# Performance work log

Hardware: AMD Instinct MI355X
Metric: run time of the kernel (lower is better)

## Reference

```python
import jax, jax.numpy as jnp
import numpy as np

B, H, S, D = 2, 12, 1024, 128
KQ, KK = 6, 11  # per-head conv kernel over (query, key) score plane


def setup_inputs() -> dict:
    key = jax.random.key(0)
    kq, kk, kv, kw = jax.random.split(key, 4)
    Q = jax.random.normal(kq, (B, H, S, D), dtype=jnp.float32)
    K = jax.random.normal(kk, (B, H, S, D), dtype=jnp.float32)
    V = jax.random.normal(kv, (B, H, S, D), dtype=jnp.float32)
    W = jax.random.normal(kw, (H, KQ, KK), dtype=jnp.float32) * 0.1
    return {"Q": Q, "K": K, "V": V, "W": W}


def reference(Q, K, V, W):
    # causal=True, softmax_scale = 1/sqrt(head_dim)  (module defaults)
    b, h, s, d = Q.shape
    _, kq, kk = W.shape
    pad_q = kq - 1            # causal padding along the query axis
    pad_k = (kk - 1) // 2     # 'same' padding along the key axis
    scale = 1.0 / np.sqrt(d).astype(np.float32)

    # Raw QK^T scores: [b, h, s_q, s_k]
    scores = jnp.einsum('bhqd,bhkd->bhqk', Q, K)

    # Causal: zero out future keys before the conv so the kernel cannot mix
    # in future information (matches the `causal` flag passed into the
    # fused qk_conv kernel; out-of-range tiles load as 0 in the Triton code).
    tril = jnp.tril(jnp.ones((s, s), dtype=bool))
    scores = jnp.where(tril[None, None], scores, 0.0)

    # Per-head 2D conv over the (q, k) plane: grouped conv with H groups,
    # kernel W[h] applied to head h's score map. Cross-correlation (PyTorch
    # conv semantics == lax.conv_general_dilated without kernel flip).
    conv = jax.lax.conv_general_dilated(
        scores,                      # [b, h, s, s] as NCHW
        W[:, None, :, :],            # [h, 1, kq, kk] as OIHW, groups=h
        window_strides=(1, 1),
        padding=((pad_q, 0), (pad_k, pad_k)),
        feature_group_count=h,
        dimension_numbers=('NCHW', 'OIHW', 'NCHW'),
    )

    # Scale, re-apply causal mask with the kernel's -1e6 fill, softmax, @V.
    logits = conv * scale + jnp.where(tril[None, None], 0.0, -1000000.0)
    P = jax.nn.softmax(logits, axis=-1)
    O = jnp.einsum('bhqk,bhkd->bhqd', P, V)
    return O
```

## Files before the change

### kernel.cpp

```cpp
#include <hip/hip_runtime.h>
#include <hip/hip_bf16.h>
#include <math.h>

#define B_ 2
#define H_ 12
#define S_ 1024
#define D_ 128
#define TQ 32
#define TK 32
#define NW 4
#define SCALE 0.08838834764831843f

#define QPAD 16
#define QROWS (S_ + QPAD)
#define KPAD 16
#define KROWS (KPAD + S_ + 16)

typedef __attribute__((ext_vector_type(8))) short short8;
typedef __attribute__((ext_vector_type(4))) float floatx4;

__device__ __forceinline__ float b2f(short s) {
    unsigned int x = ((unsigned int)(unsigned short)s) << 16;
    return __builtin_bit_cast(float, x);
}
__device__ __forceinline__ unsigned short f2b(float f) {
    return __builtin_bit_cast(unsigned short, __float2bfloat16(f));
}

__global__ __launch_bounds__(256) void cvt_pad_kernel(
    const float* __restrict__ src, unsigned short* __restrict__ dst,
    int rows_total)
{
    int idx = blockIdx.x * 256 + threadIdx.x;
    size_t e0 = (size_t)idx * 4;
    int bh = (int)(e0 / ((size_t)rows_total * D_));
    int rem = (int)(e0 - (size_t)bh * rows_total * D_);
    int r = rem / D_;
    int d = rem - r * D_;
    int sr = r - 16;
    float4 v = make_float4(0.f, 0.f, 0.f, 0.f);
    if (sr >= 0 && sr < S_)
        v = *(const float4*)(src + ((size_t)bh * S_ + sr) * D_ + d);
    ushort4 o;
    o.x = f2b(v.x); o.y = f2b(v.y); o.z = f2b(v.z); o.w = f2b(v.w);
    *(ushort4*)(dst + ((size_t)bh * rows_total + r) * D_ + d) = o;
}

__global__ __launch_bounds__(256) void vt_kernel(
    const float* __restrict__ V, unsigned short* __restrict__ Vt)
{
    __shared__ float ls[32][33];
    int b = blockIdx.x;
    int dt = b & 3; int kt = (b >> 2) & 31; int bh = b >> 7;
    int t = threadIdx.x;
    int lk = t >> 3, ld = (t & 7) * 4;
    float4 v = *(const float4*)(V + ((size_t)bh * S_ + kt * 32 + lk) * D_ + dt * 32 + ld);
    ls[lk][ld + 0] = v.x; ls[lk][ld + 1] = v.y; ls[lk][ld + 2] = v.z; ls[lk][ld + 3] = v.w;
    __syncthreads();
    int lk2 = t >> 3, lc = (t & 7) * 4;
    ushort4 o;
    o.x = f2b(ls[lc + 0][lk2]); o.y = f2b(ls[lc + 1][lk2]);
    o.z = f2b(ls[lc + 2][lk2]); o.w = f2b(ls[lc + 3][lk2]);
    *(ushort4*)(Vt + ((size_t)bh * D_ + dt * 32 + lk2) * S_ + kt * 32 + lc) = o;
}

__global__ __launch_bounds__(256, 2) void conv_attn_mfma(
    const unsigned short* __restrict__ Qp,
    const unsigned short* __restrict__ Kp,
    const unsigned short* __restrict__ Vt,
    const float* __restrict__ W,
    float* __restrict__ O)
{
    __shared__ __align__(16) union {
        unsigned short sc[NW][48][72];
        float oacc[32][132];
    } u;
    __shared__ float m_all[NW][32], l_all[NW][32], ms_s[32], inv_s[32];

    const int tid = threadIdx.x;
    const int wv = tid >> 6;
    const int ln = tid & 63;
    const int l15 = ln & 15;
    const int qd = ln >> 4;

    const int bid = blockIdx.x;
    const int bh = bid % (B_ * H_);
    const int qt = (S_ / TQ - 1) - bid / (B_ * H_);
    const int h = bh % H_;
    const int q0 = qt * TQ;

    const unsigned short* Qb = Qp + (size_t)bh * QROWS * D_;
    const unsigned short* Kb = Kp + (size_t)bh * KROWS * D_;
    const unsigned short* Vb = Vt + (size_t)bh * D_ * S_;
    const float* Wh = W + h * 66;

    short8 qf[3][4];
    #pragma unroll
    for (int mt = 0; mt < 3; ++mt) {
        const unsigned short* row = Qb + (size_t)(q0 + mt * 16 + l15) * D_;
        #pragma unroll
        for (int kc = 0; kc < 4; ++kc)
            qf[mt][kc] = *(const short8*)(row + kc * 32 + qd * 8);
    }

    floatx4 acc[2][8];
    #pragma unroll
    for (int mt = 0; mt < 2; ++mt)
        #pragma unroll
        for (int nt = 0; nt < 8; ++nt)
            acc[mt][nt] = (floatx4){0.f, 0.f, 0.f, 0.f};
    float m_run[2] = {-INFINITY, -INFINITY};
    float l_run[2] = {0.f, 0.f};

    const int nkt = qt + 1;
    for (int kt = wv; kt < nkt; kt += NW) {
        const int k0 = kt * TK;

        short8 vf[8];
        #pragma unroll
        for (int nt = 0; nt < 8; ++nt)
            vf[nt] = *(const short8*)(Vb + (size_t)(nt * 16 + l15) * S_ + k0 + qd * 8);

        #pragma unroll
        for (int nt = 0; nt < 3; ++nt) {
            const unsigned short* krow = Kb + (size_t)(k0 + 8 + nt * 16 + l15) * D_;
            short8 kf[4];
            #pragma unroll
            for (int kc = 0; kc < 4; ++kc)
                kf[kc] = *(const short8*)(krow + kc * 32 + qd * 8);
            #pragma unroll
            for (int mt = 0; mt < 3; ++mt) {
                floatx4 s = {0.f, 0.f, 0.f, 0.f};
                #pragma unroll
                for (int kc = 0; kc < 4; ++kc)
                    s = __builtin_amdgcn_mfma_f32_16x16x32_bf16(qf[mt][kc], kf[kc], s, 0, 0, 0);
                const int qrow = q0 - 16 + mt * 16 + qd * 4;
                const int kcol = k0 - 8 + nt * 16 + l15;
                #pragma unroll
                for (int reg = 0; reg < 4; ++reg) {
                    float v = (kcol <= qrow + reg) ? s[reg] : 0.f;
                    u.sc[wv][mt * 16 + qd * 4 + reg][nt * 16 + l15] = f2b(v);
                }
            }
        }

        float pl[2][8];
        #pragma unroll
        for (int mt2 = 0; mt2 < 2; ++mt2)
            #pragma unroll
            for (int jj = 0; jj < 8; ++jj) pl[mt2][jj] = 0.f;
        #pragma unroll
        for (int i = 0; i < 6; ++i) {
            const unsigned short* r0 = &u.sc[wv][l15 + 11 + i][qd * 8];
            const unsigned short* r1 = &u.sc[wv][l15 + 27 + i][qd * 8];
            short8 h0 = *(const short8*)(r0);
            short8 h1 = *(const short8*)(r0 + 8);
            short8 h2 = *(const short8*)(r0 + 16);
            short8 g0 = *(const short8*)(r1);
            short8 g1 = *(const short8*)(r1 + 8);
            short8 g2 = *(const short8*)(r1 + 16);
            float x0[24], x1[24];
            #pragma unroll
            for (int m = 0; m < 8; ++m) {
                x0[m] = b2f(h0[m]); x0[8 + m] = b2f(h1[m]); x0[16 + m] = b2f(h2[m]);
                x1[m] = b2f(g0[m]); x1[8 + m] = b2f(g1[m]); x1[16 + m] = b2f(g2[m]);
            }
            #pragma unroll
            for (int j = 0; j < 11; ++j) {
                const float w = Wh[i * 11 + j];
                #pragma unroll
                for (int jj = 0; jj < 8; ++jj) {
                    pl[0][jj] += w * x0[3 + j + jj];
                    pl[1][jj] += w * x1[3 + j + jj];
                }
            }
        }

        float al[2];
        short8 pfrag[2];
        #pragma unroll
        for (int mt2 = 0; mt2 < 2; ++mt2) {
            const int qrow = q0 + l15 + 16 * mt2;
            float lg[8];
            float mx = -1e30f;
            #pragma unroll
            for (int jj = 0; jj < 8; ++jj) {
                const int kcol = k0 + qd * 8 + jj;
                lg[jj] = (kcol <= qrow) ? pl[mt2][jj] * SCALE : -1e30f;
                mx = fmaxf(mx, lg[jj]);
            }
            mx = fmaxf(mx, __shfl_xor(mx, 16));
            mx = fmaxf(mx, __shfl_xor(mx, 32));
            const float nm = fmaxf(m_run[mt2], mx);
            al[mt2] = __expf(m_run[mt2] - nm);
            float sum = 0.f;
            short8 pb;
            #pragma unroll
            for (int jj = 0; jj < 8; ++jj) {
                float p = __expf(lg[jj] - nm);
                sum += p;
                pb[jj] = (short)f2b(p);
            }
            sum += __shfl_xor(sum, 16);
            sum += __shfl_xor(sum, 32);
            l_run[mt2] = l_run[mt2] * al[mt2] + sum;
            m_run[mt2] = nm;
            pfrag[mt2] = pb;
        }

        #pragma unroll
        for (int mt = 0; mt < 2; ++mt) {
            #pragma unroll
            for (int reg = 0; reg < 4; ++reg) {
                const float af = __shfl(al[mt], qd * 4 + reg, 64);
                #pragma unroll
                for (int nt = 0; nt < 8; ++nt)
                    acc[mt][nt][reg] *= af;
            }
        }

        #pragma unroll
        for (int nt = 0; nt < 8; ++nt)
            #pragma unroll
            for (int mt = 0; mt < 2; ++mt)
                acc[mt][nt] = __builtin_amdgcn_mfma_f32_16x16x32_bf16(pfrag[mt], vf[nt], acc[mt][nt], 0, 0, 0);
    }

    if (qd == 0) {
        m_all[wv][l15] = m_run[0]; m_all[wv][l15 + 16] = m_run[1];
        l_all[wv][l15] = l_run[0]; l_all[wv][l15 + 16] = l_run[1];
    }
    __syncthreads();
    if (tid < 32) {
        float ms = -INFINITY;
        #pragma unroll
        for (int w = 0; w < NW; ++w) ms = fmaxf(ms, m_all[w][tid]);
        float ls = 0.f;
        #pragma unroll
        for (int w = 0; w < NW; ++w) ls += __expf(m_all[w][tid] - ms) * l_all[w][tid];
        ms_s[tid] = ms;
        inv_s[tid] = 1.f / ls;
    }
    __syncthreads();
    for (int w = 0; w < NW; ++w) {
        if (wv == w) {
            #pragma unroll
            for (int mt = 0; mt < 2; ++mt) {
                #pragma unroll
                for (int reg = 0; reg < 4; ++reg) {
                    const int row = mt * 16 + qd * 4 + reg;
                    const float f = __expf(m_all[wv][row] - ms_s[row]);
                    #pragma unroll
                    for (int nt = 0; nt < 8; ++nt) {
                        const float val = acc[mt][nt][reg] * f;
                        if (w == 0) u.oacc[row][nt * 16 + l15] = val;
                        else        u.oacc[row][nt * 16 + l15] += val;
                    }
                }
            }
        }
        __syncthreads();
    }

    {
        const int r = tid >> 3;
        const int c0 = (tid & 7) * 16;
        const float inv = inv_s[r];
        float* orow = O + ((size_t)bh * S_ + q0 + r) * D_ + c0;
        #pragma unroll
        for (int g = 0; g < 4; ++g) {
            float4 o;
            o.x = u.oacc[r][c0 + g * 4 + 0] * inv;
            o.y = u.oacc[r][c0 + g * 4 + 1] * inv;
            o.z = u.oacc[r][c0 + g * 4 + 2] * inv;
            o.w = u.oacc[r][c0 + g * 4 + 3] * inv;
            *(float4*)(orow + g * 4) = o;
        }
    }
}

extern "C" void kernel_launch(void* const* d_in, const int* in_sizes, int n_in,
                              void* d_out, int out_size, void* d_ws, size_t ws_size,
                              hipStream_t stream) {
    const float* Q = (const float*)d_in[0];
    const float* K = (const float*)d_in[1];
    const float* V = (const float*)d_in[2];
    const float* W = (const float*)d_in[3];
    float* O = (float*)d_out;

    unsigned short* Qp = (unsigned short*)d_ws;
    unsigned short* Kp = (unsigned short*)((char*)d_ws + 6389760);
    unsigned short* Vt = (unsigned short*)((char*)d_ws + 12877824);

    cvt_pad_kernel<<<dim3((B_ * H_ * QROWS * D_) / 1024), dim3(256), 0, stream>>>(Q, Qp, QROWS);
    cvt_pad_kernel<<<dim3((B_ * H_ * KROWS * D_) / 1024), dim3(256), 0, stream>>>(K, Kp, KROWS);
    vt_kernel<<<dim3(B_ * H_ * (S_ / 32) * (D_ / 32)), dim3(256), 0, stream>>>(V, Vt);

    conv_attn_mfma<<<dim3(B_ * H_ * (S_ / TQ)), dim3(256), 0, stream>>>(Qp, Kp, Vt, W, O);
}
```

Before: 200.7 us.

## Fold per-head conv weights into K, turning conv-attention into a wide matmul

The kernel now absorbs the (q,k) conv into a precomputed 6x-wide key tensor: each key row is convolved with the head's weights along the key axis for each query offset, so the score becomes one MFMA GEMM over a 768-wide contraction with shifted Q rows. Because zeroing the future entries before the conv does not factor out this way, a small correction band (diagonal offsets 0..10) is precomputed from fp32 Q·K dot products and subtracted on the near-diagonal tiles. This removes the per-tile LDS score staging and the scalar conv FMAs. In exchange it adds a large prep pass that writes a 6x-expanded K and more global traffic in the main loop. The three prep kernels are merged into one launch, and block-to-tile mapping and V layout are permuted.

```diff
diff --git a/kernel.cpp b/kernel.cpp
--- a/kernel.cpp
+++ b/kernel.cpp
@@ -6,6 +6,7 @@
 #define H_ 12
 #define S_ 1024
 #define D_ 128
+#define BH_ (B_ * H_)
 #define TQ 32
 #define TK 32
 #define NW 4
@@ -13,68 +14,127 @@
 
 #define QPAD 16
 #define QROWS (S_ + QPAD)
-#define KPAD 16
-#define KROWS (KPAD + S_ + 16)
+#define KHD 768
+
+#define NB_KH   18432
+#define NB_QP   3120
+#define NB_VT   3072
+#define NB_CORR 384
+#define NB_PREP (NB_KH + NB_QP + NB_VT + NB_CORR)
 
 typedef __attribute__((ext_vector_type(8))) short short8;
 typedef __attribute__((ext_vector_type(4))) float floatx4;
 
-__device__ __forceinline__ float b2f(short s) {
-    unsigned int x = ((unsigned int)(unsigned short)s) << 16;
-    return __builtin_bit_cast(float, x);
-}
 __device__ __forceinline__ unsigned short f2b(float f) {
     return __builtin_bit_cast(unsigned short, __float2bfloat16(f));
 }
 
-__global__ __launch_bounds__(256) void cvt_pad_kernel(
-    const float* __restrict__ src, unsigned short* __restrict__ dst,
-    int rows_total)
+__global__ __launch_bounds__(256) void prep_kernel(
+    const float* __restrict__ Q, const float* __restrict__ K,
+    const float* __restrict__ V, const float* __restrict__ W,
+    unsigned short* __restrict__ Qp, unsigned short* __restrict__ Kh,
+    unsigned short* __restrict__ Vp, float* __restrict__ Corr)
 {
-    int idx = blockIdx.x * 256 + threadIdx.x;
-    size_t e0 = (size_t)idx * 4;
-    int bh = (int)(e0 / ((size_t)rows_total * D_));
-    int rem = (int)(e0 - (size_t)bh * rows_total * D_);
-    int r = rem / D_;
-    int d = rem - r * D_;
-    int sr = r - 16;
-    float4 v = make_float4(0.f, 0.f, 0.f, 0.f);
-    if (sr >= 0 && sr < S_)
-        v = *(const float4*)(src + ((size_t)bh * S_ + sr) * D_ + d);
-    ushort4 o;
-    o.x = f2b(v.x); o.y = f2b(v.y); o.z = f2b(v.z); o.w = f2b(v.w);
-    *(ushort4*)(dst + ((size_t)bh * rows_total + r) * D_ + d) = o;
-}
-
-__global__ __launch_bounds__(256) void vt_kernel(
-    const float* __restrict__ V, unsigned short* __restrict__ Vt)
-{
-    __shared__ float ls[32][33];
-    int b = blockIdx.x;
-    int dt = b & 3; int kt = (b >> 2) & 31; int bh = b >> 7;
-    int t = threadIdx.x;
-    int lk = t >> 3, ld = (t & 7) * 4;
-    float4 v = *(const float4*)(V + ((size_t)bh * S_ + kt * 32 + lk) * D_ + dt * 32 + ld);
-    ls[lk][ld + 0] = v.x; ls[lk][ld + 1] = v.y; ls[lk][ld + 2] = v.z; ls[lk][ld + 3] = v.w;
-    __syncthreads();
-    int lk2 = t >> 3, lc = (t & 7) * 4;
-    ushort4 o;
-    o.x = f2b(ls[lc + 0][lk2]); o.y = f2b(ls[lc + 1][lk2]);
-    o.z = f2b(ls[lc + 2][lk2]); o.w = f2b(ls[lc + 3][lk2]);
-    *(ushort4*)(Vt + ((size_t)bh * D_ + dt * 32 + lk2) * S_ + kt * 32 + lc) = o;
+    __shared__ union {
+        float vt_ls[32][33];
+        float band[69][16];
+    } sm;
+    const int blk = blockIdx.x;
+    const int tid = threadIdx.x;
+
+    if (blk < NB_KH) {
+        const int idx = blk * 256 + tid;
+        const int d4 = idx & 31;
+        const int t2 = idx >> 5;
+        const int i  = t2 % 6;
+        const int t3 = t2 / 6;
+        const int k  = t3 & (S_ - 1);
+        const int bh = t3 >> 10;
+        const int h  = bh % H_;
+        const float* Kb = K + (size_t)bh * S_ * D_ + d4 * 4;
+        const float* wrow = W + h * 66 + i * 11;
+        float ax = 0.f, ay = 0.f, az = 0.f, aw = 0.f;
+        #pragma unroll
+        for (int j = 0; j < 11; ++j) {
+            const int kr = k + j - 5;
+            if (kr >= 0 && kr < S_) {
+                const float w = wrow[j] * SCALE;
+                const float4 kv = *(const float4*)(Kb + (size_t)kr * D_);
+                ax += w * kv.x; ay += w * kv.y; az += w * kv.z; aw += w * kv.w;
+            }
+        }
+        ushort4 o; o.x = f2b(ax); o.y = f2b(ay); o.z = f2b(az); o.w = f2b(aw);
+        *(ushort4*)(Kh + (((size_t)bh * S_ + k) * 6 + i) * D_ + d4 * 4) = o;
+    } else if (blk < NB_KH + NB_QP) {
+        const int idx = (blk - NB_KH) * 256 + tid;
+        const size_t e0 = (size_t)idx * 4;
+        const int bh = (int)(e0 / ((size_t)QROWS * D_));
+        const int rem = (int)(e0 - (size_t)bh * QROWS * D_);
+        const int r = rem / D_;
+        const int d = rem - r * D_;
+        const int sr = r - QPAD;
+        float4 v = make_float4(0.f, 0.f, 0.f, 0.f);
+        if (sr >= 0 && sr < S_)
+            v = *(const float4*)(Q + ((size_t)bh * S_ + sr) * D_ + d);
+        ushort4 o; o.x = f2b(v.x); o.y = f2b(v.y); o.z = f2b(v.z); o.w = f2b(v.w);
+        *(ushort4*)(Qp + ((size_t)bh * QROWS + r) * D_ + d) = o;
+    } else if (blk < NB_KH + NB_QP + NB_VT) {
+        const int b2 = blk - (NB_KH + NB_QP);
+        const int dt = b2 & 3, ktl = (b2 >> 2) & 31, bh = b2 >> 7;
+        const int lk = tid >> 3, ld = (tid & 7) * 4;
+        const float4 v4 = *(const float4*)(V + ((size_t)bh * S_ + ktl * 32 + lk) * D_ + dt * 32 + ld);
+        sm.vt_ls[lk][ld + 0] = v4.x; sm.vt_ls[lk][ld + 1] = v4.y;
+        sm.vt_ls[lk][ld + 2] = v4.z; sm.vt_ls[lk][ld + 3] = v4.w;
+        __syncthreads();
+        const int lk2 = tid >> 3, lc = (tid & 7) * 4;
+        const int pb = ((lc >> 3) << 2) | (((lc >> 2) & 1) << 4);
+        ushort4 o;
+        o.x = f2b(sm.vt_ls[pb + 0][lk2]); o.y = f2b(sm.vt_ls[pb + 1][lk2]);
+        o.z = f2b(sm.vt_ls[pb + 2][lk2]); o.w = f2b(sm.vt_ls[pb + 3][lk2]);
+        *(ushort4*)(Vp + ((size_t)bh * D_ + dt * 32 + lk2) * S_ + ktl * 32 + lc) = o;
+    } else {
+        const int cb = blk - (NB_KH + NB_QP + NB_VT);
+        const int bh = cb >> 4, q0c = (cb & 15) * 64;
+        const int h = bh % H_;
+        for (int s = tid; s < 69 * 16; s += 256) {
+            const int r = s >> 4, dsl = s & 15;
+            float v = 0.f;
+            if (dsl < 10) {
+                const int qp = q0c - 5 + r, delta = dsl + 1;
+                if (qp >= 0 && qp + delta < S_) {
+                    const float4* qr = (const float4*)(Q + ((size_t)bh * S_ + qp) * D_);
+                    const float4* kr = (const float4*)(K + ((size_t)bh * S_ + qp + delta) * D_);
+                    #pragma unroll 8
+                    for (int c = 0; c < 32; ++c) {
+                        const float4 a = qr[c], b = kr[c];
+                        v += a.x * b.x + a.y * b.y + a.z * b.z + a.w * b.w;
+                    }
+                }
+            }
+            sm.band[r][dsl] = v;
+        }
+        __syncthreads();
+        for (int e = tid; e < 64 * 16; e += 256) {
+            const int ql = e >> 4, d = e & 15;
+            float v = 0.f;
+            if (d <= 10) {
+                for (int i2 = 0; i2 < 6; ++i2)
+                    for (int j = i2 + d + 1; j < 11; ++j)
+                        v += W[h * 66 + i2 * 11 + j] * SCALE * sm.band[ql + i2][j - i2 - d - 1];
+            }
+            Corr[((size_t)bh << 14) + ((size_t)(q0c + ql) << 4) + d] = v;
+        }
+    }
 }
 
 __global__ __launch_bounds__(256, 2) void conv_attn_mfma(
     const unsigned short* __restrict__ Qp,
-    const unsigned short* __restrict__ Kp,
-    const unsigned short* __restrict__ Vt,
-    const float* __restrict__ W,
+    const unsigned short* __restrict__ Kh,
+    const unsigned short* __restrict__ Vp,
+    const float* __restrict__ Corr,
     float* __restrict__ O)
 {
-    __shared__ __align__(16) union {
-        unsigned short sc[NW][48][72];
-        float oacc[32][132];
-    } u;
+    __shared__ __align__(16) float oacc[32][132];
     __shared__ float m_all[NW][32], l_all[NW][32], ms_s[32], inv_s[32];
 
     const int tid = threadIdx.x;
@@ -84,146 +144,111 @@
     const int qd = ln >> 4;
 
     const int bid = blockIdx.x;
-    const int bh = bid % (B_ * H_);
-    const int qt = (S_ / TQ - 1) - bid / (B_ * H_);
-    const int h = bh % H_;
-    const int q0 = qt * TQ;
-
-    const unsigned short* Qb = Qp + (size_t)bh * QROWS * D_;
-    const unsigned short* Kb = Kp + (size_t)bh * KROWS * D_;
-    const unsigned short* Vb = Vt + (size_t)bh * D_ * S_;
-    const float* Wh = W + h * 66;
-
-    short8 qf[3][4];
-    #pragma unroll
-    for (int mt = 0; mt < 3; ++mt) {
-        const unsigned short* row = Qb + (size_t)(q0 + mt * 16 + l15) * D_;
-        #pragma unroll
-        for (int kc = 0; kc < 4; ++kc)
-            qf[mt][kc] = *(const short8*)(row + kc * 32 + qd * 8);
-    }
+    const int wg  = (bid & 7) * 96 + (bid >> 3);
+    const int bh  = wg >> 5;
+    const int qt  = (S_ / TQ - 1) - (wg & 31);
+    const int q0  = qt * TQ;
+
+    const unsigned short* Qb0 = Qp + ((size_t)bh * QROWS + q0 + 11 + l15) * D_ + qd * 8;
+    const unsigned short* Qb1 = Qb0 + 16 * D_;
+    const unsigned short* Khb = Kh + (size_t)bh * S_ * KHD;
+    const unsigned short* Vb  = Vp + ((size_t)bh * D_ + l15) * S_ + qd * 8;
+    const float* Cb = Corr + ((size_t)bh << 14);
 
     floatx4 acc[2][8];
     #pragma unroll
     for (int mt = 0; mt < 2; ++mt)
         #pragma unroll
-        for (int nt = 0; nt < 8; ++nt)
-            acc[mt][nt] = (floatx4){0.f, 0.f, 0.f, 0.f};
+        for (int nd = 0; nd < 8; ++nd)
+            acc[mt][nd] = (floatx4){0.f, 0.f, 0.f, 0.f};
     float m_run[2] = {-INFINITY, -INFINITY};
     float l_run[2] = {0.f, 0.f};
 
-    const int nkt = qt + 1;
-    for (int kt = wv; kt < nkt; kt += NW) {
+    for (int kt = wv; kt <= qt; kt += NW) {
         const int k0 = kt * TK;
+        const unsigned short* A0 = Khb + (size_t)(k0 + l15) * KHD + qd * 8;
+        const unsigned short* A1 = A0 + 16 * KHD;
 
         short8 vf[8];
         #pragma unroll
-        for (int nt = 0; nt < 8; ++nt)
-            vf[nt] = *(const short8*)(Vb + (size_t)(nt * 16 + l15) * S_ + k0 + qd * 8);
-
-        #pragma unroll
-        for (int nt = 0; nt < 3; ++nt) {
-            const unsigned short* krow = Kb + (size_t)(k0 + 8 + nt * 16 + l15) * D_;
-            short8 kf[4];
-            #pragma unroll
-            for (int kc = 0; kc < 4; ++kc)
-                kf[kc] = *(const short8*)(krow + kc * 32 + qd * 8);
-            #pragma unroll
-            for (int mt = 0; mt < 3; ++mt) {
-                floatx4 s = {0.f, 0.f, 0.f, 0.f};
-                #pragma unroll
-                for (int kc = 0; kc < 4; ++kc)
-                    s = __builtin_amdgcn_mfma_f32_16x16x32_bf16(qf[mt][kc], kf[kc], s, 0, 0, 0);
-                const int qrow = q0 - 16 + mt * 16 + qd * 4;
-                const int kcol = k0 - 8 + nt * 16 + l15;
-                #pragma unroll
-                for (int reg = 0; reg < 4; ++reg) {
-                    float v = (kcol <= qrow + reg) ? s[reg] : 0.f;
-                    u.sc[wv][mt * 16 + qd * 4 + reg][nt * 16 + l15] = f2b(v);
-                }
-            }
-        }
-
-        float pl[2][8];
-        #pragma unroll
-        for (int mt2 = 0; mt2 < 2; ++mt2)
-            #pragma unroll
-            for (int jj = 0; jj < 8; ++jj) pl[mt2][jj] = 0.f;
-        #pragma unroll
-        for (int i = 0; i < 6; ++i) {
-            const unsigned short* r0 = &u.sc[wv][l15 + 11 + i][qd * 8];
-            const unsigned short* r1 = &u.sc[wv][l15 + 27 + i][qd * 8];
-            short8 h0 = *(const short8*)(r0);
-            short8 h1 = *(const short8*)(r0 + 8);
-            short8 h2 = *(const short8*)(r0 + 16);
-            short8 g0 = *(const short8*)(r1);
-            short8 g1 = *(const short8*)(r1 + 8);
-            short8 g2 = *(const short8*)(r1 + 16);
-            float x0[24], x1[24];
-            #pragma unroll
-            for (int m = 0; m < 8; ++m) {
-                x0[m] = b2f(h0[m]); x0[8 + m] = b2f(h1[m]); x0[16 + m] = b2f(h2[m]);
-                x1[m] = b2f(g0[m]); x1[8 + m] = b2f(g1[m]); x1[16 + m] = b2f(g2[m]);
-            }
-            #pragma unroll
-            for (int j = 0; j < 11; ++j) {
-                const float w = Wh[i * 11 + j];
-                #pragma unroll
-                for (int jj = 0; jj < 8; ++jj) {
-                    pl[0][jj] += w * x0[3 + j + jj];
-                    pl[1][jj] += w * x1[3 + j + jj];
-                }
-            }
-        }
-
+        for (int nd = 0; nd < 8; ++nd)
+            vf[nd] = *(const short8*)(Vb + (size_t)nd * 16 * S_ + k0);
+
+        floatx4 sc_[2][2];
+        #pragma unroll
+        for (int nt = 0; nt < 2; ++nt)
+            #pragma unroll
+            for (int mt = 0; mt < 2; ++mt)
+                sc_[nt][mt] = (floatx4){0.f, 0.f, 0.f, 0.f};
+
+        #pragma unroll
+        for (int c = 0; c < 24; ++c) {
+            const short8 a0 = *(const short8*)(A0 + c * 32);
+            const short8 a1 = *(const short8*)(A1 + c * 32);
+            const short8 b0 = *(const short8*)(Qb0 + (c >> 2) * D_ + (c & 3) * 32);
+            const short8 b1 = *(const short8*)(Qb1 + (c >> 2) * D_ + (c & 3) * 32);
+            sc_[0][0] = __builtin_amdgcn_mfma_f32_16x16x32_bf16(a0, b0, sc_[0][0], 0, 0, 0);
+            sc_[0][1] = __builtin_amdgcn_mfma_f32_16x16x32_bf16(a0, b1, sc_[0][1], 0, 0, 0);
+            sc_[1][0] = __builtin_amdgcn_mfma_f32_16x16x32_bf16(a1, b0, sc_[1][0], 0, 0, 0);
+            sc_[1][1] = __builtin_amdgcn_mfma_f32_16x16x32_bf16(a1, b1, sc_[1][1], 0, 0, 0);
+        }
+
+        const bool need_corr = (kt >= qt - 1);
         float al[2];
         short8 pfrag[2];
         #pragma unroll
-        for (int mt2 = 0; mt2 < 2; ++mt2) {
-            const int qrow = q0 + l15 + 16 * mt2;
+        for (int mt = 0; mt < 2; ++mt) {
+            const int qrow = q0 + mt * 16 + l15;
             float lg[8];
             float mx = -1e30f;
             #pragma unroll
-            for (int jj = 0; jj < 8; ++jj) {
-                const int kcol = k0 + qd * 8 + jj;
-                lg[jj] = (kcol <= qrow) ? pl[mt2][jj] * SCALE : -1e30f;
-                mx = fmaxf(mx, lg[jj]);
-            }
+            for (int nt = 0; nt < 2; ++nt)
+                #pragma unroll
+                for (int rg = 0; rg < 4; ++rg) {
+                    const int kcol = k0 + nt * 16 + qd * 4 + rg;
+                    float v = sc_[nt][mt][rg];
+                    if (need_corr) {
+                        const int dd = qrow - kcol;
+                        if (dd >= 0 && dd <= 10) v -= Cb[(qrow << 4) + dd];
+                    }
+                    const int jj = nt * 4 + rg;
+                    lg[jj] = (kcol <= qrow) ? v : -1e30f;
+                    mx = fmaxf(mx, lg[jj]);
+                }
             mx = fmaxf(mx, __shfl_xor(mx, 16));
             mx = fmaxf(mx, __shfl_xor(mx, 32));
-            const float nm = fmaxf(m_run[mt2], mx);
-            al[mt2] = __expf(m_run[mt2] - nm);
+            const float nm = fmaxf(m_run[mt], mx);
+            al[mt] = __expf(m_run[mt] - nm);
             float sum = 0.f;
-            short8 pb;
+            short8 pbv;
             #pragma unroll
             for (int jj = 0; jj < 8; ++jj) {
-                float p = __expf(lg[jj] - nm);
+                const float p = __expf(lg[jj] - nm);
                 sum += p;
-                pb[jj] = (short)f2b(p);
+                pbv[jj] = (short)f2b(p);
             }
             sum += __shfl_xor(sum, 16);
             sum += __shfl_xor(sum, 32);
-            l_run[mt2] = l_run[mt2] * al[mt2] + sum;
-            m_run[mt2] = nm;
-            pfrag[mt2] = pb;
-        }
-
-        #pragma unroll
-        for (int mt = 0; mt < 2; ++mt) {
-            #pragma unroll
-            for (int reg = 0; reg < 4; ++reg) {
-                const float af = __shfl(al[mt], qd * 4 + reg, 64);
+            l_run[mt] = l_run[mt] * al[mt] + sum;
+            m_run[mt] = nm;
+            pfrag[mt] = pbv;
+        }
+
+        #pragma unroll
+        for (int mt = 0; mt < 2; ++mt)
+            #pragma unroll
+            for (int rg = 0; rg < 4; ++rg) {
+                const float af = __shfl(al[mt], qd * 4 + rg, 64);
                 #pragma unroll
-                for (int nt = 0; nt < 8; ++nt)
-                    acc[mt][nt][reg] *= af;
-            }
-        }
-
-        #pragma unroll
-        for (int nt = 0; nt < 8; ++nt)
+                for (int nd = 0; nd < 8; ++nd)
+                    acc[mt][nd][rg] *= af;
+            }
+
+        #pragma unroll
+        for (int nd = 0; nd < 8; ++nd)
             #pragma unroll
             for (int mt = 0; mt < 2; ++mt)
-                acc[mt][nt] = __builtin_amdgcn_mfma_f32_16x16x32_bf16(pfrag[mt], vf[nt], acc[mt][nt], 0, 0, 0);
+                acc[mt][nd] = __builtin_amdgcn_mfma_f32_16x16x32_bf16(pfrag[mt], vf[nd], acc[mt][nd], 0, 0, 0);
     }
 
     if (qd == 0) {
@@ -247,14 +272,14 @@
             #pragma unroll
             for (int mt = 0; mt < 2; ++mt) {
                 #pragma unroll
-                for (int reg = 0; reg < 4; ++reg) {
-                    const int row = mt * 16 + qd * 4 + reg;
+                for (int rg = 0; rg < 4; ++rg) {
+                    const int row = mt * 16 + qd * 4 + rg;
                     const float f = __expf(m_all[wv][row] - ms_s[row]);
                     #pragma unroll
-                    for (int nt = 0; nt < 8; ++nt) {
-                        const float val = acc[mt][nt][reg] * f;
-                        if (w == 0) u.oacc[row][nt * 16 + l15] = val;
-                        else        u.oacc[row][nt * 16 + l15] += val;
+                    for (int nd = 0; nd < 8; ++nd) {
+                        const float val = acc[mt][nd][rg] * f;
+                        if (w == 0) oacc[row][nd * 16 + l15] = val;
+                        else        oacc[row][nd * 16 + l15] += val;
                     }
                 }
             }
@@ -270,10 +295,10 @@
         #pragma unroll
         for (int g = 0; g < 4; ++g) {
             float4 o;
-            o.x = u.oacc[r][c0 + g * 4 + 0] * inv;
-            o.y = u.oacc[r][c0 + g * 4 + 1] * inv;
-            o.z = u.oacc[r][c0 + g * 4 + 2] * inv;
-            o.w = u.oacc[r][c0 + g * 4 + 3] * inv;
+            o.x = oacc[r][c0 + g * 4 + 0] * inv;
+            o.y = oacc[r][c0 + g * 4 + 1] * inv;
+            o.z = oacc[r][c0 + g * 4 + 2] * inv;
+            o.w = oacc[r][c0 + g * 4 + 3] * inv;
             *(float4*)(orow + g * 4) = o;
         }
     }
@@ -289,12 +314,10 @@
     float* O = (float*)d_out;
 
     unsigned short* Qp = (unsigned short*)d_ws;
-    unsigned short* Kp = (unsigned short*)((char*)d_ws + 6389760);
-    unsigned short* Vt = (unsigned short*)((char*)d_ws + 12877824);
-
-    cvt_pad_kernel<<<dim3((B_ * H_ * QROWS * D_) / 1024), dim3(256), 0, stream>>>(Q, Qp, QROWS);
-    cvt_pad_kernel<<<dim3((B_ * H_ * KROWS * D_) / 1024), dim3(256), 0, stream>>>(K, Kp, KROWS);
-    vt_kernel<<<dim3(B_ * H_ * (S_ / 32) * (D_ / 32)), dim3(256), 0, stream>>>(V, Vt);
-
-    conv_attn_mfma<<<dim3(B_ * H_ * (S_ / TQ)), dim3(256), 0, stream>>>(Qp, Kp, Vt, W, O);
+    unsigned short* Kh = (unsigned short*)((char*)d_ws + 6389760);
+    unsigned short* Vp = (unsigned short*)((char*)d_ws + 44138496);
+    float*          Cr = (float*)((char*)d_ws + 50429952);
+
+    prep_kernel<<<dim3(NB_PREP), dim3(256), 0, stream>>>(Q, K, V, W, Qp, Kh, Vp, Cr);
+    conv_attn_mfma<<<dim3(BH_ * (S_ / TQ)), dim3(256), 0, stream>>>(Qp, Kh, Vp, Cr, O);
 }
```

New measurement: 418.8 us. 2.09x slower.
